# Performance work log

Measured on AMD Instinct MI355X. Metric: run time of the kernel, lower is better.

Reference implementation:

```python
import jax, jax.numpy as jnp
import numpy as np

N = 100000
E = 1600000
IN = 128
HID = 32
HEADS = 4
HID2 = 8  # hidden_channels / 4
OUT = 1


def setup_inputs() -> dict:
    key = jax.random.key(0)
    ks = jax.random.split(key, 13)
    def glorot(k, shape):
        fan = sum(shape[-2:]) if len(shape) >= 2 else shape[-1]
        return jax.random.normal(k, shape, dtype=jnp.float32) * (2.0 / fan) ** 0.5
    return {
        "x": jax.random.normal(ks[0], (N, IN), dtype=jnp.float32),
        "edge_index": jax.random.randint(ks[1], (2, E), 0, N, dtype=jnp.int32),
        "edge_attr": jax.random.normal(ks[2], (E, 8), dtype=jnp.float32),  # ignored by GATConv (edge_dim=None)
        "W1": glorot(ks[3], (IN, HEADS * HID)),
        "a_src1": glorot(ks[4], (HEADS, HID)),
        "a_dst1": glorot(ks[5], (HEADS, HID)),
        "b1": jnp.zeros((HEADS * HID,), dtype=jnp.float32),
        "W2": glorot(ks[6], (HEADS * HID, 1 * HID2)),
        "a_src2": glorot(ks[7], (1, HID2)),
        "a_dst2": glorot(ks[8], (1, HID2)),
        "b2": jnp.zeros((HID2,), dtype=jnp.float32),
        "Wlin": glorot(ks[9], (HID2, OUT)),
        "blin": jnp.zeros((OUT,), dtype=jnp.float32),
    }


def gat_layer(x, W, a_src, a_dst, bias, src, dst, num_nodes, concat):
    """PyG GATConv (edge_dim=None): gather -> LeakyReLU attn -> segment softmax over dst -> scatter-add."""
    H, C = a_src.shape
    h = (x @ W).reshape(num_nodes, H, C)                        # [N, H, C]
    alpha_s = jnp.einsum('nhc,hc->nh', h, a_src)                # [N, H]
    alpha_d = jnp.einsum('nhc,hc->nh', h, a_dst)
    e = jax.nn.leaky_relu(alpha_s[src] + alpha_d[dst], 0.2)     # [E, H]
    m = jax.ops.segment_max(e, dst, num_segments=num_nodes)     # softmax over incoming edges per dst
    ex = jnp.exp(e - m[dst])
    denom = jax.ops.segment_sum(ex, dst, num_segments=num_nodes)
    alpha = ex / (denom[dst] + 1e-16)                           # [E, H]
    out = jax.ops.segment_sum(h[src] * alpha[:, :, None], dst, num_segments=num_nodes)  # [N, H, C]
    out = out.reshape(num_nodes, H * C) if concat else out.mean(axis=1)
    return out + bias


def reference(x, edge_index, edge_attr, W1, a_src1, a_dst1, b1, W2, a_src2, a_dst2, b2, Wlin, blin):
    n = x.shape[0]
    loops = jnp.arange(n, dtype=edge_index.dtype)               # add_self_loops=True (PyG default)
    src = jnp.concatenate([edge_index[0], loops])
    dst = jnp.concatenate([edge_index[1], loops])
    h = jax.nn.elu(gat_layer(x, W1, a_src1, a_dst1, b1, src, dst, n, True))
    h = jax.nn.elu(gat_layer(h, W2, a_src2, a_dst2, b2, src, dst, n, False))
    return jax.nn.sigmoid(h @ Wlin + blin)                      # [N, 1]
```

## Files before the change

### kernel.cpp

```cpp
#include <hip/hip_runtime.h>
#include <hip/hip_bf16.h>

__device__ __forceinline__ float lrelu02(float v) { return v > 0.f ? v : 0.2f * v; }

__device__ __forceinline__ float bf2f(unsigned short u) {
    union { unsigned int i; float f; } v; v.i = ((unsigned int)u) << 16; return v.f;
}
__device__ __forceinline__ unsigned short f2bf(float f) {
    union { float f; unsigned int i; } v; v.f = f;
    unsigned int x = v.i;
    return (unsigned short)((x + 0x7fffu + ((x >> 16) & 1u)) >> 16);
}
__device__ __forceinline__ unsigned short f2h(float f) {
    union { _Float16 h; unsigned short u; } v; v.h = (_Float16)f; return v.u;
}

typedef float f32x4 __attribute__((ext_vector_type(4)));
typedef short s16x8 __attribute__((ext_vector_type(8)));

using half2v = decltype(__builtin_amdgcn_cvt_pkrtz(0.f, 0.f));

__device__ __forceinline__ half2v u2h2(unsigned int u) {
    union { unsigned int u; half2v h; } v; v.u = u; return v.h;
}
__device__ __forceinline__ unsigned int h22u(half2v h) {
    union { unsigned int u; half2v h; } v; v.h = h; return v.u;
}

__global__ __launch_bounds__(256) void rank_k(
    const int* __restrict__ ei, int E, int N,
    int* __restrict__ deg, int* __restrict__ rank)
{
    int e = blockIdx.x * 256 + threadIdx.x;
    if (e >= E + N) return;
    int d = (e < E) ? ei[E + e] : (e - E);
    rank[e] = atomicAdd(&deg[d], 1);
}

__global__ __launch_bounds__(512) void gemm1_k(
    const float* __restrict__ x, const float* __restrict__ W1,
    const float* __restrict__ aw_s, const float* __restrict__ aw_d,
    unsigned short* __restrict__ h1b, float* __restrict__ as1, float* __restrict__ ad1, int N)
{
    __shared__ unsigned short Wt[128 * 128];
    {
        const float4* W4 = (const float4*)W1;
        for (int i = threadIdx.x; i < 128 * 32; i += 512) {
            float4 f = W4[i];
            int k = i >> 5, c4 = (i & 31) * 4;
            #pragma unroll
            for (int j = 0; j < 4; ++j) {
                int col = c4 + j;
                float fv = j == 0 ? f.x : j == 1 ? f.y : j == 2 ? f.z : f.w;
                Wt[col * 128 + (k ^ ((col & 7) << 3))] = f2bf(fv);
            }
        }
    }

    const int lane = threadIdx.x & 63;
    const int wv   = threadIdx.x >> 6;
    const int li   = lane & 15;
    const int kg   = lane >> 4;
    const int row0 = blockIdx.x * 128 + wv * 16;

    const int rc = (row0 + li < N) ? (row0 + li) : (N - 1);
    const float4* xr = (const float4*)(x + (size_t)rc * 128);

    f32x4 acc[8];
    #pragma unroll
    for (int ct = 0; ct < 8; ++ct) acc[ct] = {0.f, 0.f, 0.f, 0.f};

    __syncthreads();

    #pragma unroll
    for (int ks = 0; ks < 4; ++ks) {
        float4 f0 = xr[ks * 8 + kg * 2];
        float4 f1 = xr[ks * 8 + kg * 2 + 1];
        float xf[8] = {f0.x, f0.y, f0.z, f0.w, f1.x, f1.y, f1.z, f1.w};
        s16x8 ahi, alo;
        #pragma unroll
        for (int j = 0; j < 8; ++j) {
            unsigned short h = f2bf(xf[j]);
            ahi[j] = (short)h;
            alo[j] = (short)f2bf(xf[j] - bf2f(h));
        }
        const int kbase = ks * 32 + kg * 8;
        #pragma unroll
        for (int ct = 0; ct < 8; ++ct) {
            const int col = ct * 16 + li;
            const s16x8 b = *reinterpret_cast<const s16x8*>(
                Wt + col * 128 + (kbase ^ ((col & 7) << 3)));
            acc[ct] = __builtin_amdgcn_mfma_f32_16x16x32_bf16(ahi, b, acc[ct], 0, 0, 0);
            acc[ct] = __builtin_amdgcn_mfma_f32_16x16x32_bf16(alo, b, acc[ct], 0, 0, 0);
        }
    }

    float aws_[8], awd_[8];
    #pragma unroll
    for (int t = 0; t < 8; ++t) { aws_[t] = aw_s[t * 16 + li]; awd_[t] = aw_d[t * 16 + li]; }

    #pragma unroll
    for (int i = 0; i < 4; ++i) {
        const int gr = row0 + (lane >> 4) * 4 + i;
        const bool valid = gr < N;
        float s0 = acc[0][i] * aws_[0] + acc[1][i] * aws_[1];
        float s1 = acc[2][i] * aws_[2] + acc[3][i] * aws_[3];
        float s2 = acc[4][i] * aws_[4] + acc[5][i] * aws_[5];
        float s3 = acc[6][i] * aws_[6] + acc[7][i] * aws_[7];
        float d0 = acc[0][i] * awd_[0] + acc[1][i] * awd_[1];
        float d1 = acc[2][i] * awd_[2] + acc[3][i] * awd_[3];
        float d2 = acc[4][i] * awd_[4] + acc[5][i] * awd_[5];
        float d3 = acc[6][i] * awd_[6] + acc[7][i] * awd_[7];
        #pragma unroll
        for (int m = 1; m < 16; m <<= 1) {
            s0 += __shfl_xor(s0, m, 16); s1 += __shfl_xor(s1, m, 16);
            s2 += __shfl_xor(s2, m, 16); s3 += __shfl_xor(s3, m, 16);
            d0 += __shfl_xor(d0, m, 16); d1 += __shfl_xor(d1, m, 16);
            d2 += __shfl_xor(d2, m, 16); d3 += __shfl_xor(d3, m, 16);
        }
        if (valid) {
            if (li < 4) {
                float sv = li == 0 ? s0 : li == 1 ? s1 : li == 2 ? s2 : s3;
                float dv = li == 0 ? d0 : li == 1 ? d1 : li == 2 ? d2 : d3;
                as1[gr * 4 + li] = sv;
                ad1[gr * 4 + li] = dv;
            }
            #pragma unroll
            for (int ct = 0; ct < 8; ++ct)
                h1b[(size_t)gr * 128 + ct * 16 + li] = f2h(acc[ct][i]);
        }
    }
}

__global__ __launch_bounds__(256) void blocksum_k(
    const int* __restrict__ deg, int N, int* __restrict__ bsum)
{
    __shared__ int sh[256];
    int i = blockIdx.x * 256 + threadIdx.x;
    sh[threadIdx.x] = (i < N) ? deg[i] : 0;
    __syncthreads();
    for (int off = 128; off; off >>= 1) {
        if (threadIdx.x < off) sh[threadIdx.x] += sh[threadIdx.x + off];
        __syncthreads();
    }
    if (threadIdx.x == 0) bsum[blockIdx.x] = sh[0];
}

__global__ __launch_bounds__(1024) void scanbsum_k(int* __restrict__ bsum, int nb)
{
    __shared__ int buf[1024];
    __shared__ int carry;
    if (threadIdx.x == 0) carry = 0;
    __syncthreads();
    for (int base = 0; base < nb; base += 1024) {
        int i = base + threadIdx.x;
        int v = (i < nb) ? bsum[i] : 0;
        buf[threadIdx.x] = v;
        __syncthreads();
        for (int off = 1; off < 1024; off <<= 1) {
            int t = (threadIdx.x >= off) ? buf[threadIdx.x - off] : 0;
            __syncthreads();
            buf[threadIdx.x] += t;
            __syncthreads();
        }
        if (i < nb) bsum[i] = buf[threadIdx.x] - v + carry;
        __syncthreads();
        if (threadIdx.x == 0) carry += buf[1023];
        __syncthreads();
    }
}

__global__ __launch_bounds__(256) void rowptr_k(
    const int* __restrict__ deg, const int* __restrict__ bsum, int N, int E,
    int* __restrict__ rowptr)
{
    __shared__ int buf[256];
    int i = blockIdx.x * 256 + threadIdx.x;
    int v = (i < N) ? deg[i] : 0;
    buf[threadIdx.x] = v;
    __syncthreads();
    for (int off = 1; off < 256; off <<= 1) {
        int t = (threadIdx.x >= off) ? buf[threadIdx.x - off] : 0;
        __syncthreads();
        buf[threadIdx.x] += t;
        __syncthreads();
    }
    if (i < N) rowptr[i] = bsum[blockIdx.x] + buf[threadIdx.x] - v;
    if (i == 0) rowptr[N] = E + N;
}

__global__ __launch_bounds__(256) void place_k(
    const int* __restrict__ ei, int E, int N,
    const int* __restrict__ rank, const int* __restrict__ rowptr,
    int* __restrict__ csr)
{
    int e = blockIdx.x * 256 + threadIdx.x;
    if (e >= E + N) return;
    int s, d;
    if (e < E) { s = ei[e]; d = ei[E + e]; } else { s = d = e - E; }
    csr[rowptr[d] + rank[e]] = s;
}

__global__ __launch_bounds__(256) void gat1_k(
    const int* __restrict__ csr, const int* __restrict__ rowptr,
    const float* __restrict__ as1, const float* __restrict__ ad1,
    const unsigned short* __restrict__ h1b, const float* __restrict__ b1,
    const float* __restrict__ W2, const float* __restrict__ aw_s2, const float* __restrict__ aw_d2,
    float* __restrict__ g, float* __restrict__ as2, float* __restrict__ ad2, int N)
{
    __shared__ float red[4][8][12];
    const int wv   = threadIdx.x >> 6;
    const int wid  = (blockIdx.x * 256 + threadIdx.x) >> 6;
    const int lane = threadIdx.x & 63;
    if (wid >= N) return;
    const int start = rowptr[wid], end = rowptr[wid + 1];
    const int i16 = lane & 15;
    const int hh  = lane >> 4;
    const float adh = ad1[wid * 4 + hh];
    const float mh  = lrelu02(as1[wid * 4 + hh] + adh);
    const unsigned short* hb = h1b + lane * 2;

    float den = 0.f, acc0 = 0.f, acc1 = 0.f;

    int   s = 0;
    unsigned int wpku = 0;

    auto pair_step = [&](int p) {
        const int se0 = __builtin_amdgcn_readlane(s, 2 * p);
        const int se1 = __builtin_amdgcn_readlane(s, 2 * p + 1);
        const unsigned int wp = (unsigned int)__shfl((int)wpku, 2 * p, 16);
        const unsigned int pv0 = *(const unsigned int*)(hb + (size_t)se0 * 128);
        const unsigned int pv1 = *(const unsigned int*)(hb + (size_t)se1 * 128);
        const unsigned int lo = __builtin_amdgcn_perm(pv1, pv0, 0x05040100u);
        const unsigned int hi = __builtin_amdgcn_perm(pv1, pv0, 0x07060302u);
        acc0 = __builtin_amdgcn_fdot2(u2h2(wp), u2h2(lo), acc0, false);
        acc1 = __builtin_amdgcn_fdot2(u2h2(wp), u2h2(hi), acc1, false);
    };

    int k0 = start;
    int cnt = end - k0; cnt = cnt > 16 ? 16 : cnt;
    s = (i16 < cnt) ? csr[k0 + i16] : wid;
    float w = (i16 < cnt) ? __expf(lrelu02(as1[(size_t)s * 4 + hh] + adh) - mh) : 0.f;

    while (true) {
        const int k1 = k0 + 16;
        int cnt_n = end - k1; cnt_n = cnt_n > 16 ? 16 : cnt_n;
        int   s_n = wid;
        float a_n = 0.f;
        if (cnt_n > 0) {
            s_n = (i16 < cnt_n) ? csr[k1 + i16] : wid;
            a_n = as1[(size_t)s_n * 4 + hh];
        }

        den += w;
        const float wn = __shfl_xor(w, 1);
        wpku = h22u(__builtin_amdgcn_cvt_pkrtz(w, wn));

        if (cnt == 16) {
            #pragma unroll
            for (int p = 0; p < 8; ++p) pair_step(p);
        } else {
            const int pairs = (cnt + 1) >> 1;
            for (int p = 0; p < pairs; ++p) pair_step(p);
        }
        if (cnt_n <= 0) break;
        s = s_n;
        w = (i16 < cnt_n) ? __expf(lrelu02(a_n + adh) - mh) : 0.f;
        k0 = k1; cnt = cnt_n;
    }

    den += __shfl_xor(den, 1); den += __shfl_xor(den, 2);
    den += __shfl_xor(den, 4); den += __shfl_xor(den, 8);
    const float rden = 1.f / (den + 1e-16f);
    float v0 = acc0 * rden + b1[lane * 2];
    float v1 = acc1 * rden + b1[lane * 2 + 1];
    v0 = v0 > 0.f ? v0 : expm1f(v0);
    v1 = v1 > 0.f ? v1 : expm1f(v1);

    const float4 a0 = *(const float4*)(W2 + 16 * lane);
    const float4 a1 = *(const float4*)(W2 + 16 * lane + 4);
    const float4 b0 = *(const float4*)(W2 + 16 * lane + 8);
    const float4 b1v = *(const float4*)(W2 + 16 * lane + 12);
    float p[8];
    p[0] = v0 * a0.x + v1 * b0.x;  p[1] = v0 * a0.y + v1 * b0.y;
    p[2] = v0 * a0.z + v1 * b0.z;  p[3] = v0 * a0.w + v1 * b0.w;
    p[4] = v0 * a1.x + v1 * b1v.x; p[5] = v0 * a1.y + v1 * b1v.y;
    p[6] = v0 * a1.z + v1 * b1v.z; p[7] = v0 * a1.w + v1 * b1v.w;
    #pragma unroll
    for (int j = 0; j < 8; ++j) {
        p[j] += __shfl_xor(p[j], 8);
        p[j] += __shfl_xor(p[j], 16);
        p[j] += __shfl_xor(p[j], 32);
    }
    if (lane < 8) {
        #pragma unroll
        for (int j = 0; j < 8; ++j) red[wv][lane][j] = p[j];
    }
    if (lane < 8) {
        float gj = 0.f;
        #pragma unroll
        for (int c = 0; c < 8; ++c) gj += red[wv][c][lane];
        g[(size_t)wid * 8 + lane] = gj;
        float ts = gj * aw_s2[lane], td = gj * aw_d2[lane];
        ts += __shfl_xor(ts, 1); ts += __shfl_xor(ts, 2); ts += __shfl_xor(ts, 4);
        td += __shfl_xor(td, 1); td += __shfl_xor(td, 2); td += __shfl_xor(td, 4);
        if (lane == 0) { as2[wid] = ts; ad2[wid] = td; }
    }
}

__global__ __launch_bounds__(256) void gat2_k(
    const int* __restrict__ csr, const int* __restrict__ rowptr,
    const float* __restrict__ as2, const float* __restrict__ ad2,
    const float* __restrict__ g, const float* __restrict__ b2_,
    const float* __restrict__ Wlin, const float* __restrict__ blin,
    float* __restrict__ out, int N)
{
    const int wid  = (blockIdx.x * 256 + threadIdx.x) >> 6;
    const int lane = threadIdx.x & 63;
    if (wid >= N) return;
    const int start = rowptr[wid], end = rowptr[wid + 1];
    const int i8  = lane & 7;
    const int grp = lane >> 3;
    const float adh = ad2[wid];
    const float mh  = lrelu02(as2[wid] + adh);
    float den = 0.f, acc = 0.f;

    int k0 = start;
    int cnt = end - k0; cnt = cnt > 8 ? 8 : cnt;
    int   s = (i8 < cnt) ? csr[k0 + i8] : wid;
    float w = (i8 < cnt) ? __expf(lrelu02(as2[s] + adh) - mh) : 0.f;

    while (true) {
        const int k1 = k0 + 8;
        int cnt_n = end - k1; cnt_n = cnt_n > 8 ? 8 : cnt_n;
        int   s_n = wid;
        float a_n = 0.f;
        if (cnt_n > 0) {
            s_n = (i8 < cnt_n) ? csr[k1 + i8] : wid;
            a_n = as2[s_n];
        }

        den += w;
        int   se = __shfl(s, grp, 8);
        float we = __shfl(w, grp, 8);
        acc = fmaf(we, g[(size_t)se * 8 + i8], acc);

        if (cnt_n <= 0) break;
        s = s_n;
        w = (i8 < cnt_n) ? __expf(lrelu02(a_n + adh) - mh) : 0.f;
        k0 = k1; cnt = cnt_n;
    }

    den += __shfl_xor(den, 1); den += __shfl_xor(den, 2); den += __shfl_xor(den, 4);
    acc += __shfl_xor(acc, 8); acc += __shfl_xor(acc, 16); acc += __shfl_xor(acc, 32);
    float v = acc / (den + 1e-16f) + b2_[i8];
    v = v > 0.f ? v : expm1f(v);
    float t = v * Wlin[i8];
    t += __shfl_xor(t, 1); t += __shfl_xor(t, 2); t += __shfl_xor(t, 4);
    if (lane == 0) out[wid] = 1.f / (1.f + __expf(-(t + blin[0])));
}

extern "C" void kernel_launch(void* const* d_in, const int* in_sizes, int n_in,
                              void* d_out, int out_size, void* d_ws, size_t ws_size,
                              hipStream_t stream)
{
    (void)n_in; (void)out_size; (void)ws_size;
    const float* x    = (const float*)d_in[0];
    const int*   ei   = (const int*)d_in[1];
    const float* W1   = (const float*)d_in[3];
    const float* as1w = (const float*)d_in[4];
    const float* ad1w = (const float*)d_in[5];
    const float* b1   = (const float*)d_in[6];
    const float* W2   = (const float*)d_in[7];
    const float* as2w = (const float*)d_in[8];
    const float* ad2w = (const float*)d_in[9];
    const float* b2v  = (const float*)d_in[10];
    const float* Wlin = (const float*)d_in[11];
    const float* blin = (const float*)d_in[12];

    const int N = in_sizes[0] / 128;
    const int E = in_sizes[1] / 2;
    const int total = E + N;

    float* p = (float*)d_ws;
    unsigned short* h1b = (unsigned short*)p; p += (size_t)N * 64;
    float* as1  = p; p += (size_t)N * 4;
    float* ad1  = p; p += (size_t)N * 4;
    float* g    = p; p += (size_t)N * 8;
    float* as2  = p; p += (size_t)N;
    float* ad2  = p; p += (size_t)N;
    int* deg    = (int*)p; p += (size_t)N;
    int* rowptr = (int*)p; p += (size_t)N + 1;
    int* bsum   = (int*)p; p += ((size_t)N + 255) / 256;
    int* rank   = (int*)p; p += (size_t)total;
    int* csr    = (int*)p; p += (size_t)total;

    const int eb = (total + 255) / 256;
    const int nb = (N + 255) / 256;

    hipMemsetAsync(deg, 0, (size_t)N * sizeof(int), stream);
    rank_k<<<eb, 256, 0, stream>>>(ei, E, N, deg, rank);
    gemm1_k<<<(N + 127) / 128, 512, 0, stream>>>(x, W1, as1w, ad1w, h1b, as1, ad1, N);
    blocksum_k<<<nb, 256, 0, stream>>>(deg, N, bsum);
    scanbsum_k<<<1, 1024, 0, stream>>>(bsum, nb);
    rowptr_k<<<nb, 256, 0, stream>>>(deg, bsum, N, E, rowptr);
    place_k<<<eb, 256, 0, stream>>>(ei, E, N, rank, rowptr, csr);

    gat1_k<<<(N * 64 + 255) / 256, 256, 0, stream>>>(csr, rowptr, as1, ad1, h1b, b1,
                                                     W2, as2w, ad2w, g, as2, ad2, N);
    gat2_k<<<(N * 64 + 255) / 256, 256, 0, stream>>>(csr, rowptr, as2, ad2, g, b2v, Wlin, blin,
                                                     (float*)d_out, N);
}
```

Before: 409.7 us.

## Fuse CSR construction into one cooperative kernel and widen gat2 edge batches

```diff
diff --git a/kernel.cpp b/kernel.cpp
--- a/kernel.cpp
+++ b/kernel.cpp
@@ -1,5 +1,8 @@
 #include <hip/hip_runtime.h>
 #include <hip/hip_bf16.h>
+#include <hip/hip_cooperative_groups.h>
+
+namespace cg = cooperative_groups;
 
 __device__ __forceinline__ float lrelu02(float v) { return v > 0.f ? v : 0.2f * v; }
 
@@ -27,14 +30,90 @@
     union { unsigned int u; half2v h; } v; v.h = h; return v.u;
 }
 
-__global__ __launch_bounds__(256) void rank_k(
+__global__ __launch_bounds__(256) void csr_build_k(
     const int* __restrict__ ei, int E, int N,
-    int* __restrict__ deg, int* __restrict__ rank)
+    int* __restrict__ deg, int* __restrict__ rank,
+    int* __restrict__ bsum, int* __restrict__ rowptr, int* __restrict__ csr)
 {
-    int e = blockIdx.x * 256 + threadIdx.x;
-    if (e >= E + N) return;
-    int d = (e < E) ? ei[E + e] : (e - E);
-    rank[e] = atomicAdd(&deg[d], 1);
+    cg::grid_group grid = cg::this_grid();
+    const int tid = blockIdx.x * 256 + threadIdx.x;
+    const int gstride = gridDim.x * 256;
+    const int total = E + N;
+    __shared__ int sh[256];
+    __shared__ int carry;
+
+    for (int i = tid; i < N; i += gstride) deg[i] = 0;
+    __threadfence();
+    grid.sync();
+
+    for (int e = tid; e < total; e += gstride) {
+        int d = (e < E) ? ei[E + e] : (e - E);
+        rank[e] = atomicAdd(&deg[d], 1);
+    }
+    __threadfence();
+    grid.sync();
+
+    const int nseg = (N + 255) / 256;
+    for (int seg = blockIdx.x; seg < nseg; seg += gridDim.x) {
+        int i = seg * 256 + threadIdx.x;
+        sh[threadIdx.x] = (i < N) ? deg[i] : 0;
+        __syncthreads();
+        for (int off = 128; off; off >>= 1) {
+            if (threadIdx.x < off) sh[threadIdx.x] += sh[threadIdx.x + off];
+            __syncthreads();
+        }
+        if (threadIdx.x == 0) bsum[seg] = sh[0];
+        __syncthreads();
+    }
+    __threadfence();
+    grid.sync();
+
+    if (blockIdx.x == 0) {
+        if (threadIdx.x == 0) carry = 0;
+        __syncthreads();
+        for (int base = 0; base < nseg; base += 256) {
+            int i = base + threadIdx.x;
+            int v = (i < nseg) ? bsum[i] : 0;
+            sh[threadIdx.x] = v;
+            __syncthreads();
+            for (int off = 1; off < 256; off <<= 1) {
+                int t = (threadIdx.x >= off) ? sh[threadIdx.x - off] : 0;
+                __syncthreads();
+                sh[threadIdx.x] += t;
+                __syncthreads();
+            }
+            if (i < nseg) bsum[i] = sh[threadIdx.x] - v + carry;
+            __syncthreads();
+            if (threadIdx.x == 0) carry += sh[255];
+            __syncthreads();
+        }
+    }
+    __threadfence();
+    grid.sync();
+
+    for (int seg = blockIdx.x; seg < nseg; seg += gridDim.x) {
+        int i = seg * 256 + threadIdx.x;
+        int v = (i < N) ? deg[i] : 0;
+        sh[threadIdx.x] = v;
+        __syncthreads();
+        for (int off = 1; off < 256; off <<= 1) {
+            int t = (threadIdx.x >= off) ? sh[threadIdx.x - off] : 0;
+            __syncthreads();
+            sh[threadIdx.x] += t;
+            __syncthreads();
+        }
+        if (i < N) rowptr[i] = bsum[seg] + sh[threadIdx.x] - v;
+        __syncthreads();
+    }
+    if (tid == 0) rowptr[N] = total;
+    __threadfence();
+    grid.sync();
+
+    for (int e = tid; e < total; e += gstride) {
+        int s, d;
+        if (e < E) { s = ei[e]; d = ei[E + e]; } else { s = d = e - E; }
+        csr[rowptr[d] + rank[e]] = s;
+    }
 }
 
 __global__ __launch_bounds__(512) void gemm1_k(
@@ -132,75 +211,6 @@
     }
 }
 
-__global__ __launch_bounds__(256) void blocksum_k(
-    const int* __restrict__ deg, int N, int* __restrict__ bsum)
-{
-    __shared__ int sh[256];
-    int i = blockIdx.x * 256 + threadIdx.x;
-    sh[threadIdx.x] = (i < N) ? deg[i] : 0;
-    __syncthreads();
-    for (int off = 128; off; off >>= 1) {
-        if (threadIdx.x < off) sh[threadIdx.x] += sh[threadIdx.x + off];
-        __syncthreads();
-    }
-    if (threadIdx.x == 0) bsum[blockIdx.x] = sh[0];
-}
-
-__global__ __launch_bounds__(1024) void scanbsum_k(int* __restrict__ bsum, int nb)
-{
-    __shared__ int buf[1024];
-    __shared__ int carry;
-    if (threadIdx.x == 0) carry = 0;
-    __syncthreads();
-    for (int base = 0; base < nb; base += 1024) {
-        int i = base + threadIdx.x;
-        int v = (i < nb) ? bsum[i] : 0;
-        buf[threadIdx.x] = v;
-        __syncthreads();
-        for (int off = 1; off < 1024; off <<= 1) {
-            int t = (threadIdx.x >= off) ? buf[threadIdx.x - off] : 0;
-            __syncthreads();
-            buf[threadIdx.x] += t;
-            __syncthreads();
-        }
-        if (i < nb) bsum[i] = buf[threadIdx.x] - v + carry;
-        __syncthreads();
-        if (threadIdx.x == 0) carry += buf[1023];
-        __syncthreads();
-    }
-}
-
-__global__ __launch_bounds__(256) void rowptr_k(
-    const int* __restrict__ deg, const int* __restrict__ bsum, int N, int E,
-    int* __restrict__ rowptr)
-{
-    __shared__ int buf[256];
-    int i = blockIdx.x * 256 + threadIdx.x;
-    int v = (i < N) ? deg[i] : 0;
-    buf[threadIdx.x] = v;
-    __syncthreads();
-    for (int off = 1; off < 256; off <<= 1) {
-        int t = (threadIdx.x >= off) ? buf[threadIdx.x - off] : 0;
-        __syncthreads();
-        buf[threadIdx.x] += t;
-        __syncthreads();
-    }
-    if (i < N) rowptr[i] = bsum[blockIdx.x] + buf[threadIdx.x] - v;
-    if (i == 0) rowptr[N] = E + N;
-}
-
-__global__ __launch_bounds__(256) void place_k(
-    const int* __restrict__ ei, int E, int N,
-    const int* __restrict__ rank, const int* __restrict__ rowptr,
-    int* __restrict__ csr)
-{
-    int e = blockIdx.x * 256 + threadIdx.x;
-    if (e >= E + N) return;
-    int s, d;
-    if (e < E) { s = ei[e]; d = ei[E + e]; } else { s = d = e - E; }
-    csr[rowptr[d] + rank[e]] = s;
-}
-
 __global__ __launch_bounds__(256) void gat1_k(
     const int* __restrict__ csr, const int* __restrict__ rowptr,
     const float* __restrict__ as1, const float* __restrict__ ad1,
@@ -319,6 +329,7 @@
     const int lane = threadIdx.x & 63;
     if (wid >= N) return;
     const int start = rowptr[wid], end = rowptr[wid + 1];
+    const int i16 = lane & 15;
     const int i8  = lane & 7;
     const int grp = lane >> 3;
     const float adh = ad2[wid];
@@ -326,32 +337,38 @@
     float den = 0.f, acc = 0.f;
 
     int k0 = start;
-    int cnt = end - k0; cnt = cnt > 8 ? 8 : cnt;
-    int   s = (i8 < cnt) ? csr[k0 + i8] : wid;
-    float w = (i8 < cnt) ? __expf(lrelu02(as2[s] + adh) - mh) : 0.f;
+    int cnt = end - k0; cnt = cnt > 16 ? 16 : cnt;
+    int   s = (i16 < cnt) ? csr[k0 + i16] : wid;
+    float w = (i16 < cnt) ? __expf(lrelu02(as2[s] + adh) - mh) : 0.f;
 
     while (true) {
-        const int k1 = k0 + 8;
-        int cnt_n = end - k1; cnt_n = cnt_n > 8 ? 8 : cnt_n;
+        const int k1 = k0 + 16;
+        int cnt_n = end - k1; cnt_n = cnt_n > 16 ? 16 : cnt_n;
         int   s_n = wid;
         float a_n = 0.f;
         if (cnt_n > 0) {
-            s_n = (i8 < cnt_n) ? csr[k1 + i8] : wid;
+            s_n = (i16 < cnt_n) ? csr[k1 + i16] : wid;
             a_n = as2[s_n];
         }
 
         den += w;
-        int   se = __shfl(s, grp, 8);
-        float we = __shfl(w, grp, 8);
-        acc = fmaf(we, g[(size_t)se * 8 + i8], acc);
+        const int   se0 = __shfl(s, grp);
+        const int   se1 = __shfl(s, grp + 8);
+        const float we0 = __shfl(w, grp);
+        const float we1 = __shfl(w, grp + 8);
+        const float gv0 = g[(size_t)se0 * 8 + i8];
+        const float gv1 = g[(size_t)se1 * 8 + i8];
+        acc = fmaf(we0, gv0, acc);
+        acc = fmaf(we1, gv1, acc);
 
         if (cnt_n <= 0) break;
         s = s_n;
-        w = (i8 < cnt_n) ? __expf(lrelu02(a_n + adh) - mh) : 0.f;
+        w = (i16 < cnt_n) ? __expf(lrelu02(a_n + adh) - mh) : 0.f;
         k0 = k1; cnt = cnt_n;
     }
 
-    den += __shfl_xor(den, 1); den += __shfl_xor(den, 2); den += __shfl_xor(den, 4);
+    den += __shfl_xor(den, 1); den += __shfl_xor(den, 2);
+    den += __shfl_xor(den, 4); den += __shfl_xor(den, 8);
     acc += __shfl_xor(acc, 8); acc += __shfl_xor(acc, 16); acc += __shfl_xor(acc, 32);
     float v = acc / (den + 1e-16f) + b2_[i8];
     v = v > 0.f ? v : expm1f(v);
@@ -395,16 +412,15 @@
     int* rank   = (int*)p; p += (size_t)total;
     int* csr    = (int*)p; p += (size_t)total;
 
-    const int eb = (total + 255) / 256;
-    const int nb = (N + 255) / 256;
-
-    hipMemsetAsync(deg, 0, (size_t)N * sizeof(int), stream);
-    rank_k<<<eb, 256, 0, stream>>>(ei, E, N, deg, rank);
     gemm1_k<<<(N + 127) / 128, 512, 0, stream>>>(x, W1, as1w, ad1w, h1b, as1, ad1, N);
-    blocksum_k<<<nb, 256, 0, stream>>>(deg, N, bsum);
-    scanbsum_k<<<1, 1024, 0, stream>>>(bsum, nb);
-    rowptr_k<<<nb, 256, 0, stream>>>(deg, bsum, N, E, rowptr);
-    place_k<<<eb, 256, 0, stream>>>(ei, E, N, rank, rowptr, csr);
+
+    {
+        int* ei_nc = (int*)ei;
+        void* args[] = { (void*)&ei_nc, (void*)&E, (void*)&N, (void*)&deg,
+                         (void*)&rank, (void*)&bsum, (void*)&rowptr, (void*)&csr };
+        hipLaunchCooperativeKernel((void*)csr_build_k, dim3(1024), dim3(256),
+                                   args, 0, stream);
+    }
 
     gat1_k<<<(N * 64 + 255) / 256, 256, 0, stream>>>(csr, rowptr, as1, ad1, h1b, b1,
                                                      W2, as2w, ad2w, g, as2, ad2, N);
```

New measurement: 1.191 ms. 2.91x slower.
